# Kernel optimization log

Measured on AMD Instinct MI355X. Metric: run time of the kernel, lower is better.

The kernel has to match this reference:

```python
import jax, jax.numpy as jnp
import numpy as np
from jax import lax

DROP_PROB = 0.1
BLOCK_SIZE = 7
FEAT_SIZE = 56
GAMMA = DROP_PROB / BLOCK_SIZE ** 2 * (FEAT_SIZE ** 2 / (FEAT_SIZE - BLOCK_SIZE + 1) ** 2)


def setup_inputs() -> dict:
    key = jax.random.key(0)
    k1, k2 = jax.random.split(key)
    x = jax.random.normal(k1, (32, 256, 56, 56), dtype=jnp.float32)
    u = jax.random.uniform(k2, (56, 56), dtype=jnp.float32)
    return {"x": x, "u": u}


def reference(x, u):
    # Bernoulli(gamma) seed mask over (H, W)
    mask = (u < GAMMA).astype(x.dtype)
    # Original code scatters 1s at seed + offsets in [0, block)^2 (down/right),
    # then crops to (H, W). Equivalent: backward-looking max window of size block.
    dilated = lax.reduce_window(
        mask, jnp.array(0.0, x.dtype), lax.max,
        window_dimensions=(BLOCK_SIZE, BLOCK_SIZE),
        window_strides=(1, 1),
        padding=((BLOCK_SIZE - 1, 0), (BLOCK_SIZE - 1, 0)),
    )
    block_mask = 1.0 - dilated  # (H, W), 0 inside dropped blocks
    scale = block_mask.size / jnp.sum(block_mask)
    return x * block_mask[None, None, :, :] * scale
```

## Files before the change

kernel.cpp:

```cpp
#include <hip/hip_runtime.h>


#define HW    3136
#define WDIM  56
#define HDIM  56
#define HW4   784
#define ROWMASK 0x00FFFFFFFFFFFFFFull

typedef float vfloat4 __attribute__((ext_vector_type(4)));

__global__ void __launch_bounds__(256) dropblock_mask_kernel(
        const float* __restrict__ u, float* __restrict__ m) {
    __shared__ unsigned char seed[HW];
    __shared__ unsigned long long rowdil[HDIM];
    __shared__ unsigned long long dropbits[HDIM];
    __shared__ int rowkept[HDIM];
    __shared__ float s_scale;

    const float gamma = (float)(0.1 / 49.0 * (3136.0 / 2500.0));

    for (int i = threadIdx.x; i < HW; i += 256)
        seed[i] = (u[i] < gamma) ? (unsigned char)1 : (unsigned char)0;
    __syncthreads();

    if (threadIdx.x < 64) {
        int r = threadIdx.x;
        if (r < HDIM) {
            unsigned long long rowmask = 0ull;
            const unsigned char* srow = &seed[r * WDIM];
            #pragma unroll
            for (int c = 0; c < WDIM; ++c)
                rowmask |= ((unsigned long long)srow[c]) << c;
            unsigned long long rd = rowmask;
            #pragma unroll
            for (int k = 1; k < 7; ++k) rd |= (rowmask << k);
            rd &= ROWMASK;
            rowdil[r] = rd;
        }
        __builtin_amdgcn_wave_barrier();
        if (r < HDIM) {
            int j0 = (r >= 6) ? r - 6 : 0;
            unsigned long long d = 0ull;
            for (int j = j0; j <= r; ++j) d |= rowdil[j];
            d &= ROWMASK;
            dropbits[r] = d;
            rowkept[r] = WDIM - __popcll(d);
        }
    }
    __syncthreads();

    if (threadIdx.x == 0) {
        int total = 0;
        for (int r = 0; r < HDIM; ++r) total += rowkept[r];
        s_scale = (float)HW / (float)total;
    }
    __syncthreads();

    float scale = s_scale;
    for (int i = threadIdx.x; i < HW; i += 256) {
        int r = i / WDIM, c = i % WDIM;
        m[i] = ((dropbits[r] >> c) & 1ull) ? 0.0f : scale;
    }
}

__global__ void __launch_bounds__(256) dropblock_apply_kernel(
        const vfloat4* __restrict__ x, const vfloat4* __restrict__ m4,
        vfloat4* __restrict__ out, unsigned int nvec) {
    unsigned int i = blockIdx.x * 256u + threadIdx.x;
    if (i >= nvec) return;
    unsigned int p = i % (unsigned int)HW4;
    vfloat4 xv = __builtin_nontemporal_load(&x[i]);
    vfloat4 mv = m4[p];
    vfloat4 o = xv * mv;
    __builtin_nontemporal_store(o, &out[i]);
}

extern "C" void kernel_launch(void* const* d_in, const int* in_sizes, int n_in,
                              void* d_out, int out_size, void* d_ws, size_t ws_size,
                              hipStream_t stream) {
    const float* x = (const float*)d_in[0];
    const float* u = (const float*)d_in[1];
    float* out = (float*)d_out;
    float* m   = (float*)d_ws;

    dropblock_mask_kernel<<<1, 256, 0, stream>>>(u, m);

    unsigned int nvec = (unsigned int)(out_size / 4);
    unsigned int blocks = (nvec + 255u) / 256u;
    dropblock_apply_kernel<<<blocks, 256, 0, stream>>>(
        (const vfloat4*)x, (const vfloat4*)m, (vfloat4*)out, nvec);
}
```

Before: 181.7 us.

## Fuse mask computation into persistent grid-stride apply kernel with LDS mask

Merges the single-block mask kernel into the apply kernel. Each of 2048 persistent blocks recomputes the dropblock mask into shared memory and then grid-strides over x, reading the mask from LDS instead of global memory. This removes one kernel launch and the serialized single-block dependency. In exchange, every block redundantly does the mask computation and uses about 16KB of extra LDS, which may limit occupancy.

```diff
diff --git a/kernel.cpp b/kernel.cpp
--- a/kernel.cpp
+++ b/kernel.cpp
@@ -6,16 +6,21 @@
 #define HDIM  56
 #define HW4   784
 #define ROWMASK 0x00FFFFFFFFFFFFFFull
+#define NBLOCKS 2048
+#define STRIDE  (NBLOCKS * 256u)
+#define PSTEP   576u
 
 typedef float vfloat4 __attribute__((ext_vector_type(4)));
 
-__global__ void __launch_bounds__(256) dropblock_mask_kernel(
-        const float* __restrict__ u, float* __restrict__ m) {
+__global__ void __launch_bounds__(256) dropblock_fused_kernel(
+        const float* __restrict__ u, const vfloat4* __restrict__ x,
+        vfloat4* __restrict__ out, unsigned int nvec) {
     __shared__ unsigned char seed[HW];
     __shared__ unsigned long long rowdil[HDIM];
     __shared__ unsigned long long dropbits[HDIM];
     __shared__ int rowkept[HDIM];
     __shared__ float s_scale;
+    __shared__ vfloat4 m4s[HW4];
 
     const float gamma = (float)(0.1 / 49.0 * (3136.0 / 2500.0));
 
@@ -56,23 +61,25 @@
     }
     __syncthreads();
 
-    float scale = s_scale;
-    for (int i = threadIdx.x; i < HW; i += 256) {
-        int r = i / WDIM, c = i % WDIM;
-        m[i] = ((dropbits[r] >> c) & 1ull) ? 0.0f : scale;
+    {
+        float scale = s_scale;
+        float* mf = (float*)m4s;
+        for (int i = threadIdx.x; i < HW; i += 256) {
+            int r = i / WDIM, c = i % WDIM;
+            mf[i] = ((dropbits[r] >> c) & 1ull) ? 0.0f : scale;
+        }
     }
-}
+    __syncthreads();
 
-__global__ void __launch_bounds__(256) dropblock_apply_kernel(
-        const vfloat4* __restrict__ x, const vfloat4* __restrict__ m4,
-        vfloat4* __restrict__ out, unsigned int nvec) {
     unsigned int i = blockIdx.x * 256u + threadIdx.x;
-    if (i >= nvec) return;
     unsigned int p = i % (unsigned int)HW4;
-    vfloat4 xv = __builtin_nontemporal_load(&x[i]);
-    vfloat4 mv = m4[p];
-    vfloat4 o = xv * mv;
-    __builtin_nontemporal_store(o, &out[i]);
+    for (; i < nvec; i += STRIDE) {
+        vfloat4 xv = __builtin_nontemporal_load(&x[i]);
+        vfloat4 o = xv * m4s[p];
+        __builtin_nontemporal_store(o, &out[i]);
+        p += PSTEP;
+        if (p >= (unsigned int)HW4) p -= (unsigned int)HW4;
+    }
 }
 
 extern "C" void kernel_launch(void* const* d_in, const int* in_sizes, int n_in,
@@ -81,12 +88,8 @@
     const float* x = (const float*)d_in[0];
     const float* u = (const float*)d_in[1];
     float* out = (float*)d_out;
-    float* m   = (float*)d_ws;
-
-    dropblock_mask_kernel<<<1, 256, 0, stream>>>(u, m);
 
     unsigned int nvec = (unsigned int)(out_size / 4);
-    unsigned int blocks = (nvec + 255u) / 256u;
-    dropblock_apply_kernel<<<blocks, 256, 0, stream>>>(
-        (const vfloat4*)x, (const vfloat4*)m, (vfloat4*)out, nvec);
+    dropblock_fused_kernel<<<NBLOCKS, 256, 0, stream>>>(
+        u, (const vfloat4*)x, (vfloat4*)out, nvec);
 }
```

New measurement: 180.0 us. No clear change (-1.0%).
